# Performance work log

Hardware: AMD Instinct MI355X
Metric: run time of the kernel (lower is better)

The kernel has to match this reference:

```python
import jax, jax.numpy as jnp
import numpy as np

P = 16         # patch size
D = 192        # embed dim (vit_tiny)
NH = 3         # heads
DEPTH = 12
HID = 768      # mlp hidden = 4*D
NCLS = 1000
PCT = 0.25
EPS = 1e-6


def _ln(x, s, b):
    m = x.mean(-1, keepdims=True)
    v = ((x - m) ** 2).mean(-1, keepdims=True)
    return (x - m) * jax.lax.rsqrt(v + EPS) * s + b


def setup_inputs() -> dict:
    key = jax.random.key(0)
    ks = jax.random.split(key, 24)
    B, IMG = 64, 384
    std = 0.02
    d = {
        "magno_image": jax.random.normal(ks[0], (B, 3, IMG, IMG), jnp.float32),
        "line_drawing": jax.random.uniform(ks[1], (B, 1, IMG, IMG), jnp.float32),
        "conv_w": jax.random.normal(ks[2], (D, 3, P, P), jnp.float32) * std,
        "conv_b": jnp.zeros((D,), jnp.float32),
        "pos_embed": jax.random.normal(ks[3], (1, (IMG // P) ** 2 + 1, D), jnp.float32) * std,
        "cls_token": jax.random.normal(ks[4], (1, 1, D), jnp.float32) * std,
        "ln1_s": jnp.ones((DEPTH, D), jnp.float32),
        "ln1_b": jnp.zeros((DEPTH, D), jnp.float32),
        "qkv_w": jax.random.normal(ks[5], (DEPTH, D, 3 * D), jnp.float32) * std,
        "qkv_b": jnp.zeros((DEPTH, 3 * D), jnp.float32),
        "proj_w": jax.random.normal(ks[6], (DEPTH, D, D), jnp.float32) * std,
        "proj_b": jnp.zeros((DEPTH, D), jnp.float32),
        "ln2_s": jnp.ones((DEPTH, D), jnp.float32),
        "ln2_b": jnp.zeros((DEPTH, D), jnp.float32),
        "fc1_w": jax.random.normal(ks[7], (DEPTH, D, HID), jnp.float32) * std,
        "fc1_b": jnp.zeros((DEPTH, HID), jnp.float32),
        "fc2_w": jax.random.normal(ks[8], (DEPTH, HID, D), jnp.float32) * std,
        "fc2_b": jnp.zeros((DEPTH, D), jnp.float32),
        "normf_s": jnp.ones((D,), jnp.float32),
        "normf_b": jnp.zeros((D,), jnp.float32),
        "head_w": jax.random.normal(ks[9], (D, NCLS), jnp.float32) * std,
        "head_b": jnp.zeros((NCLS,), jnp.float32),
    }
    return d


def _forward(magno_image, line_drawing, conv_w, conv_b, pos_embed, cls_token,
             ln1_s, ln1_b, qkv_w, qkv_b, proj_w, proj_b, ln2_s, ln2_b,
             fc1_w, fc1_b, fc2_w, fc2_b, normf_s, normf_b, head_w, head_b):
    B, _, IMG, _ = magno_image.shape
    g = IMG // P
    N = g * g
    k = int(N * PCT)
    hd = D // NH

    # --- PatchImportanceScorer: avg-pool(patch_size) then flatten ---
    scores = line_drawing.reshape(B, g, P, g, P).mean(axis=(2, 4)).reshape(B, N)

    # --- patch embed (conv stride == kernel == reshaped matmul) ---
    x = magno_image.reshape(B, 3, g, P, g, P).transpose(0, 2, 4, 1, 3, 5)
    patches = x.reshape(B, N, 3 * P * P) @ conv_w.reshape(D, 3 * P * P).T + conv_b

    # --- top_k selection + gather of patches and pos-embed ---
    _, idx = jax.lax.top_k(scores, k)                      # (B, k)
    sel = jnp.take_along_axis(patches, idx[:, :, None], axis=1)
    pos = jnp.take_along_axis(
        jnp.broadcast_to(pos_embed[:, 1:, :], (B, N, D)), idx[:, :, None], axis=1)
    sel = sel + pos

    cls = jnp.broadcast_to(cls_token + pos_embed[:, :1, :], (B, 1, D))
    seq = jnp.concatenate([cls, sel], axis=1)              # (B, 1+k, D)
    S = 1 + k

    def block(h, p):
        l1s, l1b, qw, qb, pw, pb, l2s, l2b, f1w, f1b, f2w, f2b = p
        y = _ln(h, l1s, l1b)
        qkv = (y @ qw + qb).reshape(B, S, 3, NH, hd)
        q, kk, v = qkv[:, :, 0], qkv[:, :, 1], qkv[:, :, 2]  # (B,S,NH,hd)
        att = jnp.einsum('bqhd,bkhd->bhqk', q, kk) / np.sqrt(hd).astype(np.float32)
        att = jax.nn.softmax(att, axis=-1)
        o = jnp.einsum('bhqk,bkhd->bqhd', att, v).reshape(B, S, D)
        h = h + o @ pw + pb
        y = _ln(h, l2s, l2b)
        h = h + jax.nn.gelu(y @ f1w + f1b, approximate=False) @ f2w + f2b
        return h, None

    seq, _ = jax.lax.scan(block, seq, (ln1_s, ln1_b, qkv_w, qkv_b, proj_w, proj_b,
                                       ln2_s, ln2_b, fc1_w, fc1_b, fc2_w, fc2_b))
    seq = _ln(seq, normf_s, normf_b)
    return seq[:, 0] @ head_w + head_b


def reference(magno_image, line_drawing, conv_w, conv_b, pos_embed, cls_token,
              ln1_s, ln1_b, qkv_w, qkv_b, proj_w, proj_b, ln2_s, ln2_b,
              fc1_w, fc1_b, fc2_w, fc2_b, normf_s, normf_b, head_w, head_b):
    return _forward(magno_image, line_drawing, conv_w, conv_b, pos_embed, cls_token,
                    ln1_s, ln1_b, qkv_w, qkv_b, proj_w, proj_b, ln2_s, ln2_b,
                    fc1_w, fc1_b, fc2_w, fc2_b, normf_s, normf_b, head_w, head_b)
```

## Files before the change

### kernel.cpp

```cpp
#include <hip/hip_runtime.h>
#include <hip/hip_bf16.h>
#include <cmath>


#define Bsz   64
#define NPATCH 576
#define KSEL  144
#define SEQ   145
#define DIM   192
#define HIDN  768

typedef __bf16 bf16x8 __attribute__((ext_vector_type(8)));
typedef float  f32x4  __attribute__((ext_vector_type(4)));

__global__ __launch_bounds__(256) void scores_kernel(const float* __restrict__ line,
                                                     float* __restrict__ scores)
{
    int gp = blockIdx.x;
    int b = gp / NPATCH, p = gp % NPATCH;
    int gy = p / 24, gx = p % 24;
    int t = threadIdx.x, py = t >> 4, px = t & 15;
    float v = line[((size_t)b * 384 + gy * 16 + py) * 384 + gx * 16 + px];
    for (int off = 32; off; off >>= 1) v += __shfl_xor(v, off);
    __shared__ float red[4];
    if ((t & 63) == 0) red[t >> 6] = v;
    __syncthreads();
    if (t == 0) scores[gp] = (red[0] + red[1] + red[2] + red[3]) * (1.f / 256.f);
}

__global__ __launch_bounds__(256) void topk_kernel(const float* __restrict__ scores,
                                                   int* __restrict__ idx)
{
    int b = blockIdx.x;
    __shared__ float s[NPATCH];
    for (int i = threadIdx.x; i < NPATCH; i += 256) s[i] = scores[b * NPATCH + i];
    __syncthreads();
    for (int i = threadIdx.x; i < NPATCH; i += 256) {
        float si = s[i];
        int cnt = 0;
        for (int j = 0; j < NPATCH; ++j) {
            float sj = s[j];
            cnt += (sj > si) || (sj == si && j < i);
        }
        if (cnt < KSEL) idx[b * KSEL + cnt] = i;
    }
}

__global__ __launch_bounds__(256) void gather_kernel(const float* __restrict__ magno,
                                                     const int* __restrict__ idx,
                                                     __hip_bfloat16* __restrict__ selp)
{
    int bs = blockIdx.x;
    int b = bs / KSEL;
    int pi = idx[bs];
    int gy = pi / 24, gx = pi % 24;
    int t = threadIdx.x, py = t >> 4, px = t & 15;
    size_t src = ((size_t)b * 3 * 384 + gy * 16 + py) * 384 + gx * 16 + px;
    __hip_bfloat16* dst = &selp[(size_t)bs * 768];
#pragma unroll
    for (int c = 0; c < 3; ++c)
        dst[c * 256 + t] = __float2bfloat16(magno[src + (size_t)c * 384 * 384]);
}

__global__ __launch_bounds__(256) void convert_bf16_kernel(const float* __restrict__ src,
                                                           __hip_bfloat16* __restrict__ dst,
                                                           int n)
{
    int i = blockIdx.x * 256 + threadIdx.x;
    if (i < n) dst[i] = __float2bfloat16(src[i]);
}

__global__ __launch_bounds__(256) void transpose_w_kernel(const float* __restrict__ src,
                                                          __hip_bfloat16* __restrict__ dst,
                                                          int R, int C)
{
    __shared__ float t[32][33];
    size_t lo = (size_t)blockIdx.z * R * C;
    int r0 = blockIdx.y * 32, c0 = blockIdx.x * 32;
    int tx = threadIdx.x & 31, ty = threadIdx.x >> 5;
#pragma unroll
    for (int i = 0; i < 32; i += 8)
        t[ty + i][tx] = src[lo + (size_t)(r0 + ty + i) * C + c0 + tx];
    __syncthreads();
#pragma unroll
    for (int i = 0; i < 32; i += 8)
        dst[lo + (size_t)(c0 + ty + i) * R + r0 + tx] = __float2bfloat16(t[tx][ty + i]);
}

__global__ void cls_kernel(const float* __restrict__ cls, const float* __restrict__ pos,
                           float* __restrict__ h)
{
    int b = blockIdx.x, t = threadIdx.x;
    h[(size_t)b * SEQ * DIM + t] = cls[t] + pos[t];
}

__global__ __launch_bounds__(256) void ln_kernel(const float* __restrict__ x,
                                                 const float* __restrict__ s,
                                                 const float* __restrict__ bia,
                                                 __hip_bfloat16* __restrict__ y, int ntok)
{
    int w = threadIdx.x >> 6, lane = threadIdx.x & 63;
    int tok = blockIdx.x * 4 + w;
    if (tok >= ntok) return;
    const float* xp = &x[(size_t)tok * DIM];
    float x0 = xp[lane], x1 = xp[lane + 64], x2 = xp[lane + 128];
    float sum = x0 + x1 + x2;
    for (int off = 32; off; off >>= 1) sum += __shfl_xor(sum, off);
    float mean = sum * (1.f / 192.f);
    float d0 = x0 - mean, d1 = x1 - mean, d2 = x2 - mean;
    float vs = d0 * d0 + d1 * d1 + d2 * d2;
    for (int off = 32; off; off >>= 1) vs += __shfl_xor(vs, off);
    float rs = rsqrtf(vs * (1.f / 192.f) + 1e-6f);
    __hip_bfloat16* yp = &y[(size_t)tok * DIM];
    yp[lane]       = __float2bfloat16(d0 * rs * s[lane]       + bia[lane]);
    yp[lane + 64]  = __float2bfloat16(d1 * rs * s[lane + 64]  + bia[lane + 64]);
    yp[lane + 128] = __float2bfloat16(d2 * rs * s[lane + 128] + bia[lane + 128]);
}

template <int MODE>
__global__ __launch_bounds__(256) void gemm_bf16(const __hip_bfloat16* __restrict__ A,
                                                 const __hip_bfloat16* __restrict__ Wt,
                                                 const float* __restrict__ bias,
                                                 void* __restrict__ Cout,
                                                 int M, int N, int K,
                                                 const int* __restrict__ selidx,
                                                 const float* __restrict__ pos)
{
    __shared__ __align__(16) char As[8192];
    __shared__ __align__(16) char Bs[8192];
    const int tid = threadIdx.x;
    const int lane = tid & 63, wid = tid >> 6;
    const int wr = wid >> 1, wc = wid & 1;
    const int lr = lane & 15, lk = lane >> 4;
    const int m0 = blockIdx.y * 64, n0 = blockIdx.x * 64;
    f32x4 acc[2][2] = {};

    for (int k0 = 0; k0 < K; k0 += 64) {
#pragma unroll
        for (int it = 0; it < 2; ++it) {
            int chunk = it * 256 + tid;
            int r = chunk >> 3, g = chunk & 7;
            int loff = r * 128 + ((g ^ (r & 7)) * 16);
            *reinterpret_cast<uint4*>(As + loff) =
                *reinterpret_cast<const uint4*>(&A[(size_t)(m0 + r) * K + k0 + g * 8]);
            *reinterpret_cast<uint4*>(Bs + loff) =
                *reinterpret_cast<const uint4*>(&Wt[(size_t)(n0 + r) * K + k0 + g * 8]);
        }
        __syncthreads();
#pragma unroll
        for (int kc = 0; kc < 2; ++kc) {
            int g = kc * 4 + lk;
            bf16x8 af[2], bfr[2];
#pragma unroll
            for (int mi = 0; mi < 2; ++mi) {
                int r = wr * 32 + mi * 16 + lr;
                af[mi] = *reinterpret_cast<const bf16x8*>(As + r * 128 + ((g ^ (r & 7)) * 16));
            }
#pragma unroll
            for (int ni = 0; ni < 2; ++ni) {
                int r = wc * 32 + ni * 16 + lr;
                bfr[ni] = *reinterpret_cast<const bf16x8*>(Bs + r * 128 + ((g ^ (r & 7)) * 16));
            }
#pragma unroll
            for (int mi = 0; mi < 2; ++mi)
#pragma unroll
                for (int ni = 0; ni < 2; ++ni)
                    acc[mi][ni] = __builtin_amdgcn_mfma_f32_16x16x32_bf16(
                        af[mi], bfr[ni], acc[mi][ni], 0, 0, 0);
        }
        __syncthreads();
    }

#pragma unroll
    for (int mi = 0; mi < 2; ++mi)
#pragma unroll
    for (int ni = 0; ni < 2; ++ni)
#pragma unroll
    for (int j = 0; j < 4; ++j) {
        int row = m0 + wr * 32 + mi * 16 + (lane >> 4) * 4 + j;
        int col = n0 + wc * 32 + ni * 16 + (lane & 15);
        float v = acc[mi][ni][j] + bias[col];
        if (MODE == 2) {
            ((__hip_bfloat16*)Cout)[(size_t)row * N + col] =
                __float2bfloat16(0.5f * v * (1.f + erff(v * 0.70710678118654752f)));
        } else {
            int bb2 = row / KSEL, ss = row % KSEL;
            int pi = selidx[row];
            v += pos[(size_t)(1 + pi) * DIM + col];
            ((float*)Cout)[((size_t)bb2 * SEQ + 1 + ss) * DIM + col] = v;
        }
    }
}

__global__ __launch_bounds__(256) void gemm_qkv(const __hip_bfloat16* __restrict__ A,
                                                const __hip_bfloat16* __restrict__ Wt,
                                                const float* __restrict__ bias,
                                                __hip_bfloat16* __restrict__ qk,
                                                __hip_bfloat16* __restrict__ Vt)
{
    __shared__ __align__(16) char As[8192];
    __shared__ __align__(16) char Bs[8192];
    const int tid = threadIdx.x;
    const int lane = tid & 63, wid = tid >> 6;
    const int wr = wid >> 1, wc = wid & 1;
    const int lr = lane & 15, lk = lane >> 4;
    const int m0 = blockIdx.y * 64, n0 = blockIdx.x * 64;
    const int K = DIM;
    f32x4 acc[2][2] = {};

    for (int k0 = 0; k0 < K; k0 += 64) {
#pragma unroll
        for (int it = 0; it < 2; ++it) {
            int chunk = it * 256 + tid;
            int r = chunk >> 3, g = chunk & 7;
            int loff = r * 128 + ((g ^ (r & 7)) * 16);
            *reinterpret_cast<uint4*>(As + loff) =
                *reinterpret_cast<const uint4*>(&A[(size_t)(m0 + r) * K + k0 + g * 8]);
            *reinterpret_cast<uint4*>(Bs + loff) =
                *reinterpret_cast<const uint4*>(&Wt[(size_t)(n0 + r) * K + k0 + g * 8]);
        }
        __syncthreads();
#pragma unroll
        for (int kc = 0; kc < 2; ++kc) {
            int g = kc * 4 + lk;
            bf16x8 af[2], bfr[2];
#pragma unroll
            for (int mi = 0; mi < 2; ++mi) {
                int r = wr * 32 + mi * 16 + lr;
                af[mi] = *reinterpret_cast<const bf16x8*>(As + r * 128 + ((g ^ (r & 7)) * 16));
            }
#pragma unroll
            for (int ni = 0; ni < 2; ++ni) {
                int r = wc * 32 + ni * 16 + lr;
                bfr[ni] = *reinterpret_cast<const bf16x8*>(Bs + r * 128 + ((g ^ (r & 7)) * 16));
            }
#pragma unroll
            for (int mi = 0; mi < 2; ++mi)
#pragma unroll
                for (int ni = 0; ni < 2; ++ni)
                    acc[mi][ni] = __builtin_amdgcn_mfma_f32_16x16x32_bf16(
                        af[mi], bfr[ni], acc[mi][ni], 0, 0, 0);
        }
        __syncthreads();
    }

#pragma unroll
    for (int mi = 0; mi < 2; ++mi)
#pragma unroll
    for (int ni = 0; ni < 2; ++ni)
#pragma unroll
    for (int j = 0; j < 4; ++j) {
        int row = m0 + wr * 32 + mi * 16 + (lane >> 4) * 4 + j;
        int col = n0 + wc * 32 + ni * 16 + (lane & 15);
        float v = acc[mi][ni][j] + bias[col];
        if (col < 384) {
            qk[(size_t)row * 384 + col] = __float2bfloat16(v);
        } else {
            int c = col - 384;
            int b = row / SEQ, s = row - b * SEQ;
            Vt[((size_t)(b * 3 + (c >> 6)) * 64 + (c & 63)) * 160 + s] = __float2bfloat16(v);
        }
    }
}

__global__ __launch_bounds__(256) void attnproj_kernel(const __hip_bfloat16* __restrict__ qk,
                                                       const __hip_bfloat16* __restrict__ Vt,
                                                       const __hip_bfloat16* __restrict__ Wp,
                                                       const float* __restrict__ pbias,
                                                       float* __restrict__ h,
                                                       const float* __restrict__ ls,
                                                       const float* __restrict__ lb,
                                                       __hip_bfloat16* __restrict__ y)
{
    const int b = blockIdx.y, qt = blockIdx.x;
    const int tid = threadIdx.x;
    const int w = tid >> 6, lane = tid & 63;
    const int lr = lane & 15, lg = lane >> 4;
    __shared__ __hip_bfloat16 Ps[3][32][168];
    __shared__ __hip_bfloat16 Ot[32][200];
    __shared__ float redsum[4][32];
    __shared__ float redsq[4][32];

    const size_t qbase = (size_t)b * SEQ * 384;
    const int q0 = qt * 32;

    if (w < 3) {
        const int hh = w;
        bf16x8 aq[2][2];
#pragma unroll
        for (int mi = 0; mi < 2; ++mi)
#pragma unroll
            for (int ks = 0; ks < 2; ++ks)
                aq[mi][ks] = *reinterpret_cast<const bf16x8*>(
                    &qk[qbase + (size_t)(q0 + mi * 16 + lr) * 384 + hh * 64 + ks * 32 + lg * 8]);
        f32x4 sc[2][10];
#pragma unroll
        for (int mi = 0; mi < 2; ++mi)
#pragma unroll
            for (int nf = 0; nf < 10; ++nf) sc[mi][nf] = (f32x4){0.f, 0.f, 0.f, 0.f};
#pragma unroll
        for (int nf = 0; nf < 10; ++nf) {
            int key = nf * 16 + lr;
#pragma unroll
            for (int ks = 0; ks < 2; ++ks) {
                bf16x8 bk = *reinterpret_cast<const bf16x8*>(
                    &qk[qbase + (size_t)key * 384 + 192 + hh * 64 + ks * 32 + lg * 8]);
#pragma unroll
                for (int mi = 0; mi < 2; ++mi)
                    sc[mi][nf] = __builtin_amdgcn_mfma_f32_16x16x32_bf16(
                        aq[mi][ks], bk, sc[mi][nf], 0, 0, 0);
            }
        }
#pragma unroll
        for (int mi = 0; mi < 2; ++mi) {
            float mx[4] = {-1e30f, -1e30f, -1e30f, -1e30f};
#pragma unroll
            for (int nf = 0; nf < 10; ++nf) {
                bool valid = nf * 16 + lr < SEQ;
#pragma unroll
                for (int j = 0; j < 4; ++j) {
                    float v = valid ? sc[mi][nf][j] * 0.125f : -1e30f;
                    sc[mi][nf][j] = v;
                    mx[j] = fmaxf(mx[j], v);
                }
            }
#pragma unroll
            for (int j = 0; j < 4; ++j)
                for (int off = 1; off < 16; off <<= 1)
                    mx[j] = fmaxf(mx[j], __shfl_xor(mx[j], off));
            float sm[4] = {0.f, 0.f, 0.f, 0.f};
#pragma unroll
            for (int nf = 0; nf < 10; ++nf)
#pragma unroll
                for (int j = 0; j < 4; ++j) {
                    float p = __expf(sc[mi][nf][j] - mx[j]);
                    sc[mi][nf][j] = p;
                    sm[j] += p;
                }
#pragma unroll
            for (int j = 0; j < 4; ++j) {
                for (int off = 1; off < 16; off <<= 1) sm[j] += __shfl_xor(sm[j], off);
                sm[j] = 1.f / sm[j];
            }
#pragma unroll
            for (int nf = 0; nf < 10; ++nf) {
                int key = nf * 16 + lr;
#pragma unroll
                for (int j = 0; j < 4; ++j)
                    Ps[hh][mi * 16 + lg * 4 + j][key] = __float2bfloat16(sc[mi][nf][j] * sm[j]);
            }
        }
        const __hip_bfloat16* vtb = &Vt[(size_t)(b * 3 + hh) * 64 * 160];
        f32x4 oacc[2][4];
#pragma unroll
        for (int mi = 0; mi < 2; ++mi)
#pragma unroll
            for (int nf = 0; nf < 4; ++nf) oacc[mi][nf] = (f32x4){0.f, 0.f, 0.f, 0.f};
#pragma unroll
        for (int ks = 0; ks < 5; ++ks) {
            bf16x8 ap[2];
            ap[0] = *reinterpret_cast<const bf16x8*>(&Ps[hh][lr][ks * 32 + lg * 8]);
            ap[1] = *reinterpret_cast<const bf16x8*>(&Ps[hh][16 + lr][ks * 32 + lg * 8]);
#pragma unroll
            for (int nf = 0; nf < 4; ++nf) {
                bf16x8 bv = *reinterpret_cast<const bf16x8*>(
                    &vtb[(size_t)(nf * 16 + lr) * 160 + ks * 32 + lg * 8]);
#pragma unroll
                for (int mi = 0; mi < 2; ++mi)
                    oacc[mi][nf] = __builtin_amdgcn_mfma_f32_16x16x32_bf16(
                        ap[mi], bv, oacc[mi][nf], 0, 0, 0);
            }
        }
#pragma unroll
        for (int mi = 0; mi < 2; ++mi)
#pragma unroll
            for (int nf = 0; nf < 4; ++nf)
#pragma unroll
                for (int j = 0; j < 4; ++j)
                    Ot[mi * 16 + lg * 4 + j][hh * 64 + nf * 16 + lr] =
                        __float2bfloat16(oacc[mi][nf][j]);
    }
    __syncthreads();

    f32x4 pacc[2][3];
#pragma unroll
    for (int mi = 0; mi < 2; ++mi)
#pragma unroll
        for (int nf = 0; nf < 3; ++nf) pacc[mi][nf] = (f32x4){0.f, 0.f, 0.f, 0.f};
#pragma unroll
    for (int kk = 0; kk < 6; ++kk) {
        bf16x8 af[2];
        af[0] = *reinterpret_cast<const bf16x8*>(&Ot[lr][kk * 32 + lg * 8]);
        af[1] = *reinterpret_cast<const bf16x8*>(&Ot[16 + lr][kk * 32 + lg * 8]);
#pragma unroll
        for (int nf = 0; nf < 3; ++nf) {
            int ncol = w * 48 + nf * 16 + lr;
            bf16x8 bw = *reinterpret_cast<const bf16x8*>(&Wp[(size_t)ncol * 192 + kk * 32 + lg * 8]);
#pragma unroll
            for (int mi = 0; mi < 2; ++mi)
                pacc[mi][nf] = __builtin_amdgcn_mfma_f32_16x16x32_bf16(
                    af[mi], bw, pacc[mi][nf], 0, 0, 0);
        }
    }
    float v[2][3][4];
    float psum[2][4] = {}, psq[2][4] = {};
#pragma unroll
    for (int mi = 0; mi < 2; ++mi)
#pragma unroll
    for (int nf = 0; nf < 3; ++nf) {
        int col = w * 48 + nf * 16 + lr;
        float bcol = pbias[col];
#pragma unroll
        for (int j = 0; j < 4; ++j) {
            int q = q0 + mi * 16 + lg * 4 + j;
            float res = (q < SEQ) ? h[((size_t)b * SEQ + q) * DIM + col] : 0.f;
            float t = pacc[mi][nf][j] + bcol + res;
            v[mi][nf][j] = t;
            psum[mi][j] += t;
            psq[mi][j] += t * t;
        }
    }
#pragma unroll
    for (int mi = 0; mi < 2; ++mi)
#pragma unroll
        for (int j = 0; j < 4; ++j) {
            for (int off = 1; off < 16; off <<= 1) {
                psum[mi][j] += __shfl_xor(psum[mi][j], off);
                psq[mi][j]  += __shfl_xor(psq[mi][j], off);
            }
            redsum[w][mi * 16 + lg * 4 + j] = psum[mi][j];
            redsq[w][mi * 16 + lg * 4 + j]  = psq[mi][j];
        }
    __syncthreads();
#pragma unroll
    for (int mi = 0; mi < 2; ++mi) {
#pragma unroll
        for (int j = 0; j < 4; ++j) {
            int r = mi * 16 + lg * 4 + j;
            int q = q0 + r;
            if (q >= SEQ) continue;
            float tsum = redsum[0][r] + redsum[1][r] + redsum[2][r] + redsum[3][r];
            float tsq  = redsq[0][r]  + redsq[1][r]  + redsq[2][r]  + redsq[3][r];
            float mean = tsum * (1.f / 192.f);
            float var  = tsq * (1.f / 192.f) - mean * mean;
            float rs = rsqrtf(var + 1e-6f);
#pragma unroll
            for (int nf = 0; nf < 3; ++nf) {
                int col = w * 48 + nf * 16 + lr;
                float t = v[mi][nf][j];
                h[((size_t)b * SEQ + q) * DIM + col] = t;
                y[((size_t)b * SEQ + q) * DIM + col] =
                    __float2bfloat16((t - mean) * rs * ls[col] + lb[col]);
            }
        }
    }
}

template <bool DO_LN>
__global__ __launch_bounds__(256) void gemm_res_ln32(const __hip_bfloat16* __restrict__ A,
                                                     const __hip_bfloat16* __restrict__ Wt,
                                                     const float* __restrict__ bias,
                                                     float* __restrict__ h,
                                                     const float* __restrict__ ls,
                                                     const float* __restrict__ lb,
                                                     __hip_bfloat16* __restrict__ y)
{
    __shared__ __align__(16) char As[4096];
    __shared__ __align__(16) char Bs[24576];
    __shared__ float redsum[2][32];
    __shared__ float redsq[2][32];
    const int tid = threadIdx.x;
    const int lane = tid & 63, w = tid >> 6;
    const int wm = w & 1, wn = w >> 1;
    const int lr = lane & 15, lg = lane >> 4;
    const int m0 = blockIdx.x * 32;
    const int K = HIDN;
    f32x4 acc[6] = {};

    for (int k0 = 0; k0 < K; k0 += 64) {
        {
            int r = tid >> 3, g = tid & 7;
            *reinterpret_cast<uint4*>(As + r * 128 + ((g ^ (r & 7)) * 16)) =
                *reinterpret_cast<const uint4*>(&A[(size_t)(m0 + r) * K + k0 + g * 8]);
        }
        {
            int chunk = tid;
#pragma unroll
            for (int it = 0; it < 6; ++it, chunk += 256) {
                int r = chunk >> 3, g = chunk & 7;
                *reinterpret_cast<uint4*>(Bs + r * 128 + ((g ^ (r & 7)) * 16)) =
                    *reinterpret_cast<const uint4*>(&Wt[(size_t)r * K + k0 + g * 8]);
            }
        }
        __syncthreads();
#pragma unroll
        for (int kc = 0; kc < 2; ++kc) {
            int g = kc * 4 + lg;
            int ar = wm * 16 + lr;
            bf16x8 af = *reinterpret_cast<const bf16x8*>(As + ar * 128 + ((g ^ (ar & 7)) * 16));
#pragma unroll
            for (int nf = 0; nf < 6; ++nf) {
                int br = wn * 96 + nf * 16 + lr;
                bf16x8 bfv = *reinterpret_cast<const bf16x8*>(Bs + br * 128 + ((g ^ (br & 7)) * 16));
                acc[nf] = __builtin_amdgcn_mfma_f32_16x16x32_bf16(af, bfv, acc[nf], 0, 0, 0);
            }
        }
        __syncthreads();
    }

    float v[6][4];
    float sum[4] = {0.f, 0.f, 0.f, 0.f}, sq[4] = {0.f, 0.f, 0.f, 0.f};
#pragma unroll
    for (int nf = 0; nf < 6; ++nf) {
        int col = wn * 96 + nf * 16 + lr;
        float bcol = bias[col];
#pragma unroll
        for (int j = 0; j < 4; ++j) {
            int row = m0 + wm * 16 + lg * 4 + j;
            float t = acc[nf][j] + bcol + h[(size_t)row * DIM + col];
            v[nf][j] = t;
            sum[j] += t;
            sq[j] += t * t;
        }
    }
    if (DO_LN) {
#pragma unroll
        for (int j = 0; j < 4; ++j) {
            for (int off = 1; off < 16; off <<= 1) {
                sum[j] += __shfl_xor(sum[j], off);
                sq[j]  += __shfl_xor(sq[j], off);
            }
            if (lr == 0) {
                redsum[wn][wm * 16 + lg * 4 + j] = sum[j];
                redsq[wn][wm * 16 + lg * 4 + j]  = sq[j];
            }
        }
        __syncthreads();
#pragma unroll
        for (int j = 0; j < 4; ++j) {
            int r = wm * 16 + lg * 4 + j;
            int row = m0 + r;
            float tsum = redsum[0][r] + redsum[1][r];
            float tsq  = redsq[0][r]  + redsq[1][r];
            float mean = tsum * (1.f / 192.f);
            float var  = tsq * (1.f / 192.f) - mean * mean;
            float rs = rsqrtf(var + 1e-6f);
#pragma unroll
            for (int nf = 0; nf < 6; ++nf) {
                int col = wn * 96 + nf * 16 + lr;
                float t = v[nf][j];
                h[(size_t)row * DIM + col] = t;
                y[(size_t)row * DIM + col] =
                    __float2bfloat16((t - mean) * rs * ls[col] + lb[col]);
            }
        }
    } else {
#pragma unroll
        for (int nf = 0; nf < 6; ++nf) {
            int col = wn * 96 + nf * 16 + lr;
#pragma unroll
            for (int j = 0; j < 4; ++j) {
                int row = m0 + wm * 16 + lg * 4 + j;
                h[(size_t)row * DIM + col] = v[nf][j];
            }
        }
    }
}

__global__ __launch_bounds__(256) void head_kernel(const float* __restrict__ h,
                                                   const float* __restrict__ nfs,
                                                   const float* __restrict__ nfb,
                                                   const float* __restrict__ hw,
                                                   const float* __restrict__ hb,
                                                   float* __restrict__ out)
{
    int b = blockIdx.x, t = threadIdx.x;
    __shared__ float y[DIM];
    __shared__ float red[4];
    float x = (t < DIM) ? h[(size_t)b * SEQ * DIM + t] : 0.f;
    float sum = x;
    for (int off = 32; off; off >>= 1) sum += __shfl_xor(sum, off);
    if ((t & 63) == 0) red[t >> 6] = sum;
    __syncthreads();
    float mean = (red[0] + red[1] + red[2] + red[3]) * (1.f / 192.f);
    __syncthreads();
    float d = (t < DIM) ? (x - mean) : 0.f;
    float v = d * d;
    for (int off = 32; off; off >>= 1) v += __shfl_xor(v, off);
    if ((t & 63) == 0) red[t >> 6] = v;
    __syncthreads();
    float var = (red[0] + red[1] + red[2] + red[3]) * (1.f / 192.f);
    float rs = rsqrtf(var + 1e-6f);
    if (t < DIM) y[t] = d * rs * nfs[t] + nfb[t];
    __syncthreads();
    for (int n = t; n < 1000; n += 256) {
        float acc = hb[n];
#pragma unroll 8
        for (int k = 0; k < DIM; ++k)
            acc = fmaf(y[k], hw[(size_t)k * 1000 + n], acc);
        out[(size_t)b * 1000 + n] = acc;
    }
}

extern "C" void kernel_launch(void* const* d_in, const int* in_sizes, int n_in,
                              void* d_out, int out_size, void* d_ws, size_t ws_size,
                              hipStream_t stream)
{
    const float* magno  = (const float*)d_in[0];
    const float* line   = (const float*)d_in[1];
    const float* conv_w = (const float*)d_in[2];
    const float* conv_b = (const float*)d_in[3];
    const float* pos    = (const float*)d_in[4];
    const float* cls    = (const float*)d_in[5];
    const float* ln1_s  = (const float*)d_in[6];
    const float* ln1_b  = (const float*)d_in[7];
    const float* qkv_w  = (const float*)d_in[8];
    const float* qkv_b  = (const float*)d_in[9];
    const float* proj_w = (const float*)d_in[10];
    const float* proj_b = (const float*)d_in[11];
    const float* ln2_s  = (const float*)d_in[12];
    const float* ln2_b  = (const float*)d_in[13];
    const float* fc1_w  = (const float*)d_in[14];
    const float* fc1_b  = (const float*)d_in[15];
    const float* fc2_w  = (const float*)d_in[16];
    const float* fc2_b  = (const float*)d_in[17];
    const float* normf_s = (const float*)d_in[18];
    const float* normf_b = (const float*)d_in[19];
    const float* head_w = (const float*)d_in[20];
    const float* head_b = (const float*)d_in[21];
    float* out = (float*)d_out;
    (void)in_sizes; (void)n_in; (void)out_size; (void)ws_size;

    char* ws = (char*)d_ws;
    int*            idx     = (int*)            (ws + 0);
    float*          h       = (float*)          (ws + 147456);
    __hip_bfloat16* y       = (__hip_bfloat16*) (ws + 7274496);
    __hip_bfloat16* qk      = (__hip_bfloat16*) (ws + 10838016);
    __hip_bfloat16* Vt      = (__hip_bfloat16*) (ws + 17965056);
    __hip_bfloat16* tbuf    = (__hip_bfloat16*) (ws + 21897216);
    __hip_bfloat16* wt_qkv  = (__hip_bfloat16*) (ws + 36151296);
    __hip_bfloat16* wt_proj = (__hip_bfloat16*) (ws + 38805504);
    __hip_bfloat16* wt_fc1  = (__hip_bfloat16*) (ws + 39690240);
    __hip_bfloat16* wt_fc2  = (__hip_bfloat16*) (ws + 43229184);
    float*          scoresbuf = (float*)qk;
    __hip_bfloat16* convT     = y;
    __hip_bfloat16* selp      = tbuf;

    hipMemsetAsync(Vt, 0, 3932160, stream);
    transpose_w_kernel<<<dim3(18, 6, 12), 256, 0, stream>>>(qkv_w, wt_qkv, DIM, 576);
    transpose_w_kernel<<<dim3(6, 6, 12),  256, 0, stream>>>(proj_w, wt_proj, DIM, DIM);
    transpose_w_kernel<<<dim3(24, 6, 12), 256, 0, stream>>>(fc1_w, wt_fc1, DIM, HIDN);
    transpose_w_kernel<<<dim3(6, 24, 12), 256, 0, stream>>>(fc2_w, wt_fc2, HIDN, DIM);
    convert_bf16_kernel<<<576, 256, 0, stream>>>(conv_w, convT, DIM * 768);

    scores_kernel<<<Bsz * NPATCH, 256, 0, stream>>>(line, scoresbuf);
    topk_kernel<<<Bsz, 256, 0, stream>>>(scoresbuf, idx);
    gather_kernel<<<Bsz * KSEL, 256, 0, stream>>>(magno, idx, selp);
    cls_kernel<<<Bsz, DIM, 0, stream>>>(cls, pos, h);
    gemm_bf16<3><<<dim3(3, 144), 256, 0, stream>>>(selp, convT, conv_b, h,
                                                   9216, DIM, 768, idx, pos);

    const int ntok = Bsz * SEQ;
    ln_kernel<<<ntok / 4, 256, 0, stream>>>(h, ln1_s, ln1_b, y, ntok);
    for (int l = 0; l < 12; ++l) {
        gemm_qkv<<<dim3(9, 145), 256, 0, stream>>>(y, wt_qkv + (size_t)l * 576 * DIM,
                                                   qkv_b + l * 576, qk, Vt);
        attnproj_kernel<<<dim3(5, Bsz), 256, 0, stream>>>(qk, Vt,
                                                          wt_proj + (size_t)l * DIM * DIM,
                                                          proj_b + l * DIM, h,
                                                          ln2_s + l * DIM, ln2_b + l * DIM, y);
        gemm_bf16<2><<<dim3(12, 145), 256, 0, stream>>>(y, wt_fc1 + (size_t)l * HIDN * DIM,
                                                        fc1_b + l * HIDN, tbuf,
                                                        ntok, HIDN, DIM, nullptr, nullptr);
        if (l < 11)
            gemm_res_ln32<true><<<ntok / 32, 256, 0, stream>>>(
                tbuf, wt_fc2 + (size_t)l * DIM * HIDN, fc2_b + l * DIM, h,
                ln1_s + (l + 1) * DIM, ln1_b + (l + 1) * DIM, y);
        else
            gemm_res_ln32<false><<<ntok / 32, 256, 0, stream>>>(
                tbuf, wt_fc2 + (size_t)l * DIM * HIDN, fc2_b + l * DIM, h,
                nullptr, nullptr, y);
    }
    head_kernel<<<Bsz, 256, 0, stream>>>(h, normf_s, normf_b, head_w, head_b, out);
}
```

Before: 1.136 ms.

## Read GEMM weights directly from global memory instead of staging in LDS

The qkv and fc1 GEMMs, and the fc2+residual+LN GEMM, now load B-operand weight fragments straight from global memory (relying on L1/L2 cache reuse) rather than staging them through shared memory. The fc2 kernel is widened to 512 threads with 4 column-wavegroups of 48 columns, so each wave holds fewer accumulators and the LN reduction spans 4 partial sums. The generic templated GEMM is split into specialised embed and fc1 kernels. This cuts LDS traffic and footprint, which may raise occupancy, but risks uncoalesced, cache-dependent global weight reads inside the inner MFMA loop.

```diff
diff --git a/kernel.cpp b/kernel.cpp
--- a/kernel.cpp
+++ b/kernel.cpp
@@ -117,14 +117,13 @@
     yp[lane + 128] = __float2bfloat16(d2 * rs * s[lane + 128] + bia[lane + 128]);
 }
 
-template <int MODE>
-__global__ __launch_bounds__(256) void gemm_bf16(const __hip_bfloat16* __restrict__ A,
-                                                 const __hip_bfloat16* __restrict__ Wt,
-                                                 const float* __restrict__ bias,
-                                                 void* __restrict__ Cout,
-                                                 int M, int N, int K,
-                                                 const int* __restrict__ selidx,
-                                                 const float* __restrict__ pos)
+__global__ __launch_bounds__(256) void gemm_embed(const __hip_bfloat16* __restrict__ A,
+                                                  const __hip_bfloat16* __restrict__ Wt,
+                                                  const float* __restrict__ bias,
+                                                  float* __restrict__ h,
+                                                  int K,
+                                                  const int* __restrict__ selidx,
+                                                  const float* __restrict__ pos)
 {
     __shared__ __align__(16) char As[8192];
     __shared__ __align__(16) char Bs[8192];
@@ -180,15 +179,10 @@
         int row = m0 + wr * 32 + mi * 16 + (lane >> 4) * 4 + j;
         int col = n0 + wc * 32 + ni * 16 + (lane & 15);
         float v = acc[mi][ni][j] + bias[col];
-        if (MODE == 2) {
-            ((__hip_bfloat16*)Cout)[(size_t)row * N + col] =
-                __float2bfloat16(0.5f * v * (1.f + erff(v * 0.70710678118654752f)));
-        } else {
-            int bb2 = row / KSEL, ss = row % KSEL;
-            int pi = selidx[row];
-            v += pos[(size_t)(1 + pi) * DIM + col];
-            ((float*)Cout)[((size_t)bb2 * SEQ + 1 + ss) * DIM + col] = v;
-        }
+        int bb2 = row / KSEL, ss = row % KSEL;
+        int pi = selidx[row];
+        v += pos[(size_t)(1 + pi) * DIM + col];
+        h[((size_t)bb2 * SEQ + 1 + ss) * DIM + col] = v;
     }
 }
 
@@ -199,7 +193,6 @@
                                                 __hip_bfloat16* __restrict__ Vt)
 {
     __shared__ __align__(16) char As[8192];
-    __shared__ __align__(16) char Bs[8192];
     const int tid = threadIdx.x;
     const int lane = tid & 63, wid = tid >> 6;
     const int wr = wid >> 1, wc = wid & 1;
@@ -213,11 +206,8 @@
         for (int it = 0; it < 2; ++it) {
             int chunk = it * 256 + tid;
             int r = chunk >> 3, g = chunk & 7;
-            int loff = r * 128 + ((g ^ (r & 7)) * 16);
-            *reinterpret_cast<uint4*>(As + loff) =
+            *reinterpret_cast<uint4*>(As + r * 128 + ((g ^ (r & 7)) * 16)) =
                 *reinterpret_cast<const uint4*>(&A[(size_t)(m0 + r) * K + k0 + g * 8]);
-            *reinterpret_cast<uint4*>(Bs + loff) =
-                *reinterpret_cast<const uint4*>(&Wt[(size_t)(n0 + r) * K + k0 + g * 8]);
         }
         __syncthreads();
 #pragma unroll
@@ -231,8 +221,8 @@
             }
 #pragma unroll
             for (int ni = 0; ni < 2; ++ni) {
-                int r = wc * 32 + ni * 16 + lr;
-                bfr[ni] = *reinterpret_cast<const bf16x8*>(Bs + r * 128 + ((g ^ (r & 7)) * 16));
+                int col = n0 + wc * 32 + ni * 16 + lr;
+                bfr[ni] = *reinterpret_cast<const bf16x8*>(&Wt[(size_t)col * K + k0 + g * 8]);
             }
 #pragma unroll
             for (int mi = 0; mi < 2; ++mi)
@@ -263,6 +253,67 @@
     }
 }
 
+__global__ __launch_bounds__(256) void gemm_fc1(const __hip_bfloat16* __restrict__ A,
+                                                const __hip_bfloat16* __restrict__ Wt,
+                                                const float* __restrict__ bias,
+                                                __hip_bfloat16* __restrict__ Cout)
+{
+    __shared__ __align__(16) char As[8192];
+    const int tid = threadIdx.x;
+    const int lane = tid & 63, wid = tid >> 6;
+    const int wr = wid >> 1, wc = wid & 1;
+    const int lr = lane & 15, lk = lane >> 4;
+    const int m0 = blockIdx.y * 64, n0 = blockIdx.x * 64;
+    const int K = DIM, N = HIDN;
+    f32x4 acc[2][2] = {};
+
+    for (int k0 = 0; k0 < K; k0 += 64) {
+#pragma unroll
+        for (int it = 0; it < 2; ++it) {
+            int chunk = it * 256 + tid;
+            int r = chunk >> 3, g = chunk & 7;
+            *reinterpret_cast<uint4*>(As + r * 128 + ((g ^ (r & 7)) * 16)) =
+                *reinterpret_cast<const uint4*>(&A[(size_t)(m0 + r) * K + k0 + g * 8]);
+        }
+        __syncthreads();
+#pragma unroll
+        for (int kc = 0; kc < 2; ++kc) {
+            int g = kc * 4 + lk;
+            bf16x8 af[2], bfr[2];
+#pragma unroll
+            for (int mi = 0; mi < 2; ++mi) {
+                int r = wr * 32 + mi * 16 + lr;
+                af[mi] = *reinterpret_cast<const bf16x8*>(As + r * 128 + ((g ^ (r & 7)) * 16));
+            }
+#pragma unroll
+            for (int ni = 0; ni < 2; ++ni) {
+                int col = n0 + wc * 32 + ni * 16 + lr;
+                bfr[ni] = *reinterpret_cast<const bf16x8*>(&Wt[(size_t)col * K + k0 + g * 8]);
+            }
+#pragma unroll
+            for (int mi = 0; mi < 2; ++mi)
+#pragma unroll
+                for (int ni = 0; ni < 2; ++ni)
+                    acc[mi][ni] = __builtin_amdgcn_mfma_f32_16x16x32_bf16(
+                        af[mi], bfr[ni], acc[mi][ni], 0, 0, 0);
+        }
+        __syncthreads();
+    }
+
+#pragma unroll
+    for (int mi = 0; mi < 2; ++mi)
+#pragma unroll
+    for (int ni = 0; ni < 2; ++ni)
+#pragma unroll
+    for (int j = 0; j < 4; ++j) {
+        int row = m0 + wr * 32 + mi * 16 + (lane >> 4) * 4 + j;
+        int col = n0 + wc * 32 + ni * 16 + (lane & 15);
+        float v = acc[mi][ni][j] + bias[col];
+        Cout[(size_t)row * N + col] =
+            __float2bfloat16(0.5f * v * (1.f + erff(v * 0.70710678118654752f)));
+    }
+}
+
 __global__ __launch_bounds__(256) void attnproj_kernel(const __hip_bfloat16* __restrict__ qk,
                                                        const __hip_bfloat16* __restrict__ Vt,
                                                        const __hip_bfloat16* __restrict__ Wp,
@@ -457,40 +508,30 @@
 }
 
 template <bool DO_LN>
-__global__ __launch_bounds__(256) void gemm_res_ln32(const __hip_bfloat16* __restrict__ A,
-                                                     const __hip_bfloat16* __restrict__ Wt,
-                                                     const float* __restrict__ bias,
-                                                     float* __restrict__ h,
-                                                     const float* __restrict__ ls,
-                                                     const float* __restrict__ lb,
-                                                     __hip_bfloat16* __restrict__ y)
+__global__ __launch_bounds__(512) void gemm_res_ln(const __hip_bfloat16* __restrict__ A,
+                                                   const __hip_bfloat16* __restrict__ Wt,
+                                                   const float* __restrict__ bias,
+                                                   float* __restrict__ h,
+                                                   const float* __restrict__ ls,
+                                                   const float* __restrict__ lb,
+                                                   __hip_bfloat16* __restrict__ y)
 {
     __shared__ __align__(16) char As[4096];
-    __shared__ __align__(16) char Bs[24576];
-    __shared__ float redsum[2][32];
-    __shared__ float redsq[2][32];
+    __shared__ float redsum[4][32];
+    __shared__ float redsq[4][32];
     const int tid = threadIdx.x;
     const int lane = tid & 63, w = tid >> 6;
     const int wm = w & 1, wn = w >> 1;
     const int lr = lane & 15, lg = lane >> 4;
     const int m0 = blockIdx.x * 32;
     const int K = HIDN;
-    f32x4 acc[6] = {};
+    f32x4 acc[3] = {};
 
     for (int k0 = 0; k0 < K; k0 += 64) {
-        {
+        if (tid < 256) {
             int r = tid >> 3, g = tid & 7;
             *reinterpret_cast<uint4*>(As + r * 128 + ((g ^ (r & 7)) * 16)) =
                 *reinterpret_cast<const uint4*>(&A[(size_t)(m0 + r) * K + k0 + g * 8]);
-        }
-        {
-            int chunk = tid;
-#pragma unroll
-            for (int it = 0; it < 6; ++it, chunk += 256) {
-                int r = chunk >> 3, g = chunk & 7;
-                *reinterpret_cast<uint4*>(Bs + r * 128 + ((g ^ (r & 7)) * 16)) =
-                    *reinterpret_cast<const uint4*>(&Wt[(size_t)r * K + k0 + g * 8]);
-            }
         }
         __syncthreads();
 #pragma unroll
@@ -499,40 +540,40 @@
             int ar = wm * 16 + lr;
             bf16x8 af = *reinterpret_cast<const bf16x8*>(As + ar * 128 + ((g ^ (ar & 7)) * 16));
 #pragma unroll
-            for (int nf = 0; nf < 6; ++nf) {
-                int br = wn * 96 + nf * 16 + lr;
-                bf16x8 bfv = *reinterpret_cast<const bf16x8*>(Bs + br * 128 + ((g ^ (br & 7)) * 16));
-                acc[nf] = __builtin_amdgcn_mfma_f32_16x16x32_bf16(af, bfv, acc[nf], 0, 0, 0);
-            }
-        }
-        __syncthreads();
-    }
-
-    float v[6][4];
-    float sum[4] = {0.f, 0.f, 0.f, 0.f}, sq[4] = {0.f, 0.f, 0.f, 0.f};
-#pragma unroll
-    for (int nf = 0; nf < 6; ++nf) {
-        int col = wn * 96 + nf * 16 + lr;
+            for (int nf = 0; nf < 3; ++nf) {
+                int col = wn * 48 + nf * 16 + lr;
+                bf16x8 bw = *reinterpret_cast<const bf16x8*>(&Wt[(size_t)col * K + k0 + g * 8]);
+                acc[nf] = __builtin_amdgcn_mfma_f32_16x16x32_bf16(af, bw, acc[nf], 0, 0, 0);
+            }
+        }
+        __syncthreads();
+    }
+
+    float v[3][4];
+    float psum[4] = {}, psq[4] = {};
+#pragma unroll
+    for (int nf = 0; nf < 3; ++nf) {
+        int col = wn * 48 + nf * 16 + lr;
         float bcol = bias[col];
 #pragma unroll
         for (int j = 0; j < 4; ++j) {
             int row = m0 + wm * 16 + lg * 4 + j;
             float t = acc[nf][j] + bcol + h[(size_t)row * DIM + col];
             v[nf][j] = t;
-            sum[j] += t;
-            sq[j] += t * t;
+            psum[j] += t;
+            psq[j] += t * t;
         }
     }
     if (DO_LN) {
 #pragma unroll
         for (int j = 0; j < 4; ++j) {
             for (int off = 1; off < 16; off <<= 1) {
-                sum[j] += __shfl_xor(sum[j], off);
-                sq[j]  += __shfl_xor(sq[j], off);
+                psum[j] += __shfl_xor(psum[j], off);
+                psq[j]  += __shfl_xor(psq[j], off);
             }
             if (lr == 0) {
-                redsum[wn][wm * 16 + lg * 4 + j] = sum[j];
-                redsq[wn][wm * 16 + lg * 4 + j]  = sq[j];
+                redsum[wn][wm * 16 + lg * 4 + j] = psum[j];
+                redsq[wn][wm * 16 + lg * 4 + j]  = psq[j];
             }
         }
         __syncthreads();
@@ -540,14 +581,14 @@
         for (int j = 0; j < 4; ++j) {
             int r = wm * 16 + lg * 4 + j;
             int row = m0 + r;
-            float tsum = redsum[0][r] + redsum[1][r];
-            float tsq  = redsq[0][r]  + redsq[1][r];
+            float tsum = redsum[0][r] + redsum[1][r] + redsum[2][r] + redsum[3][r];
+            float tsq  = redsq[0][r]  + redsq[1][r]  + redsq[2][r]  + redsq[3][r];
             float mean = tsum * (1.f / 192.f);
             float var  = tsq * (1.f / 192.f) - mean * mean;
             float rs = rsqrtf(var + 1e-6f);
 #pragma unroll
-            for (int nf = 0; nf < 6; ++nf) {
-                int col = wn * 96 + nf * 16 + lr;
+            for (int nf = 0; nf < 3; ++nf) {
+                int col = wn * 48 + nf * 16 + lr;
                 float t = v[nf][j];
                 h[(size_t)row * DIM + col] = t;
                 y[(size_t)row * DIM + col] =
@@ -556,8 +597,8 @@
         }
     } else {
 #pragma unroll
-        for (int nf = 0; nf < 6; ++nf) {
-            int col = wn * 96 + nf * 16 + lr;
+        for (int nf = 0; nf < 3; ++nf) {
+            int col = wn * 48 + nf * 16 + lr;
 #pragma unroll
             for (int j = 0; j < 4; ++j) {
                 int row = m0 + wm * 16 + lg * 4 + j;
@@ -657,8 +698,8 @@
     topk_kernel<<<Bsz, 256, 0, stream>>>(scoresbuf, idx);
     gather_kernel<<<Bsz * KSEL, 256, 0, stream>>>(magno, idx, selp);
     cls_kernel<<<Bsz, DIM, 0, stream>>>(cls, pos, h);
-    gemm_bf16<3><<<dim3(3, 144), 256, 0, stream>>>(selp, convT, conv_b, h,
-                                                   9216, DIM, 768, idx, pos);
+    gemm_embed<<<dim3(3, 144), 256, 0, stream>>>(selp, convT, conv_b, h,
+                                                 768, idx, pos);
 
     const int ntok = Bsz * SEQ;
     ln_kernel<<<ntok / 4, 256, 0, stream>>>(h, ln1_s, ln1_b, y, ntok);
@@ -669,15 +710,14 @@
                                                           wt_proj + (size_t)l * DIM * DIM,
                                                           proj_b + l * DIM, h,
                                                           ln2_s + l * DIM, ln2_b + l * DIM, y);
-        gemm_bf16<2><<<dim3(12, 145), 256, 0, stream>>>(y, wt_fc1 + (size_t)l * HIDN * DIM,
-                                                        fc1_b + l * HIDN, tbuf,
-                                                        ntok, HIDN, DIM, nullptr, nullptr);
+        gemm_fc1<<<dim3(12, 145), 256, 0, stream>>>(y, wt_fc1 + (size_t)l * HIDN * DIM,
+                                                    fc1_b + l * HIDN, tbuf);
         if (l < 11)
-            gemm_res_ln32<true><<<ntok / 32, 256, 0, stream>>>(
+            gemm_res_ln<true><<<ntok / 32, 512, 0, stream>>>(
                 tbuf, wt_fc2 + (size_t)l * DIM * HIDN, fc2_b + l * DIM, h,
                 ln1_s + (l + 1) * DIM, ln1_b + (l + 1) * DIM, y);
         else
-            gemm_res_ln32<false><<<ntok / 32, 256, 0, stream>>>(
+            gemm_res_ln<false><<<ntok / 32, 512, 0, stream>>>(
                 tbuf, wt_fc2 + (size_t)l * DIM * HIDN, fc2_b + l * DIM, h,
                 nullptr, nullptr, y);
     }
```

Result: slower. 1.315 ms (+15.7%).
